# Kernel tuning notes

Measured on AMD Instinct MI355X. Metric: run time of the kernel, lower is better.

## Reference

```python
import jax, jax.numpy as jnp
import numpy as np

BLOCK_H = 32  # block_h from init
BLOCK_W = 32  # block_w from init


def _block_pool(mask, bh, bw):
    # mask: [H, S, S] int -> block mask [H, S//bh, S//bw] bool
    # Equivalent to the grouped Conv2d with all-ones kernel, stride=(bh,bw), then >0.
    H, S1, S2 = mask.shape
    m = mask.reshape(H, S1 // bh, bh, S2 // bw, bw).astype(jnp.float32)
    return m.sum(axis=(2, 4)) > 0


def _expand_block_mask(bm, bh, bw):
    # bm: [H, Nb_r, Nb_c] bool -> element mask [H, S, S] bool
    H, nr, nc = bm.shape
    e = jnp.broadcast_to(bm[:, :, None, :, None], (H, nr, bh, nc, bw))
    return e.reshape(H, nr * bh, nc * bw)


def setup_inputs() -> dict:
    key = jax.random.key(0)
    kq, kk, kv, km = jax.random.split(key, 4)
    Z, H, S, D = 1, 16, 2048, 64
    query = jax.random.normal(kq, (Z, H, S, D), dtype=jnp.float32)
    key_t = jax.random.normal(kk, (Z, H, S, D), dtype=jnp.float32)
    value = jax.random.normal(kv, (Z, H, S, D), dtype=jnp.float32)
    mask = jax.random.randint(km, (H, S, S), 0, 2, dtype=jnp.int32)
    return {"query": query, "key": key_t, "value": value, "mask": mask}


def reference(query, key, value, mask):
    # Dense equivalent of: sdd QK^T on layout blocks -> blocksparse causal
    # softmax (scale=1.0) -> dsd AV. Rows with no active blocks yield zeros,
    # matching the blocksparse representation (absent blocks contribute 0).
    H, S, _ = mask.shape
    bm = _block_pool(mask, BLOCK_H, BLOCK_W)              # [H, Nb, Nb]
    elem = _expand_block_mask(bm, BLOCK_H, BLOCK_W)       # [H, S, S]
    causal = jnp.tril(jnp.ones((S, S), dtype=bool))       # is_causal=True
    full = elem & causal                                  # [H, S, S]
    scale = 1.0                                           # scale=1.0 in forward

    scores = jnp.einsum('zhqd,zhkd->zhqk', query, key) * scale
    neg = jnp.asarray(-1e30, dtype=scores.dtype)
    scores = jnp.where(full[None], scores, neg)
    probs = jax.nn.softmax(scores, axis=-1)
    row_valid = jnp.any(full, axis=-1)                    # [H, S]
    probs = jnp.where(row_valid[None, :, :, None], probs, 0.0)
    out = jnp.einsum('zhqk,zhkd->zhqd', probs, value)
    return out
```

## Files before the change

### kernel.cpp

```cpp
#include <hip/hip_runtime.h>
#include <stdint.h>


#define HH 16
#define SS 2048
#define DD 64

using f32x4  = __attribute__((ext_vector_type(4))) float;
using s16x8  = __attribute__((ext_vector_type(8))) short;
using s16x4  = __attribute__((ext_vector_type(4))) short;
using f16x8  = __attribute__((ext_vector_type(8))) _Float16;

#define AS1 __attribute__((address_space(1)))
#define AS3 __attribute__((address_space(3)))

__device__ __forceinline__ unsigned short f2bf(float f) {
  unsigned u = __builtin_bit_cast(unsigned, f);
  u += 0x7fffu + ((u >> 16) & 1u);
  return (unsigned short)(u >> 16);
}
__device__ __forceinline__ float bf2f(unsigned short u) {
  return __builtin_bit_cast(float, ((unsigned)u) << 16);
}

__device__ __forceinline__ f32x4 mfma16bf16(s16x4 a, s16x4 b, f32x4 c) {
  return __builtin_amdgcn_mfma_f32_16x16x16bf16_1k(a, b, c, 0, 0, 0);
}

__global__ __launch_bounds__(256) void prep_kernel(
    const int* __restrict__ mask, const float* __restrict__ K,
    const float* __restrict__ V, unsigned char* __restrict__ bmask,
    unsigned short* __restrict__ Kf, unsigned short* __restrict__ Vtb) {
  __shared__ float tile[64][65];
  const int wg = blockIdx.x;
  const int t  = threadIdx.x;
  if (wg < 256) {
    const int tid = wg * 256 + t;
    {
      const int h = tid >> 12, br = (tid >> 6) & 63, bc = tid & 63;
      const int4* p = (const int4*)(mask + ((size_t)(h * SS + br * 32) * SS + bc * 32));
      int acc = 0;
#pragma unroll
      for (int i = 0; i < 8; ++i) { int4 v = p[i]; acc |= v.x | v.y | v.z | v.w; }
      if (acc == 0) {
        for (int r = 1; r < 32; ++r) {
          const int4* q2 = (const int4*)(mask + ((size_t)(h * SS + br * 32 + r) * SS + bc * 32));
          int a2 = 0;
#pragma unroll
          for (int i = 0; i < 8; ++i) { int4 v = q2[i]; a2 |= v.x | v.y | v.z | v.w; }
          acc |= a2;
          if (acc) break;
        }
      }
      bmask[tid] = acc != 0 ? 1 : 0;
    }
    {
      const float4* K4 = (const float4*)K;
      ushort4* Kf4 = (ushort4*)Kf;
#pragma unroll
      for (int i = 0; i < 8; ++i) {
        float4 v = K4[(size_t)i * 65536 + tid];
        ushort4 o;
        o.x = __builtin_bit_cast(unsigned short, (_Float16)v.x);
        o.y = __builtin_bit_cast(unsigned short, (_Float16)v.y);
        o.z = __builtin_bit_cast(unsigned short, (_Float16)v.z);
        o.w = __builtin_bit_cast(unsigned short, (_Float16)v.w);
        Kf4[(size_t)i * 65536 + tid] = o;
      }
    }
  } else {
    const int w2 = wg - 256;
    const int h = w2 >> 5, kt = w2 & 31;
    const float4* V4 = (const float4*)V;
#pragma unroll
    for (int j2 = 0; j2 < 4; ++j2) {
      int fi = t + j2 * 256;
      int row = fi >> 4, c4 = (fi & 15) * 4;
      float4 v = V4[(size_t)(h * SS + kt * 64 + row) * 16 + (fi & 15)];
      tile[row][c4] = v.x; tile[row][c4+1] = v.y; tile[row][c4+2] = v.z; tile[row][c4+3] = v.w;
    }
    __syncthreads();
    const int d = t >> 2, ks = (t & 3) * 16;
#pragma unroll
    for (int c = 0; c < 4; ++c) {
      ushort4 o;
      o.x = f2bf(tile[ks + c*4 + 0][d]);
      o.y = f2bf(tile[ks + c*4 + 1][d]);
      o.z = f2bf(tile[ks + c*4 + 2][d]);
      o.w = f2bf(tile[ks + c*4 + 3][d]);
      ((ushort4*)Vtb)[((size_t)(h * 64 + d) * SS + kt * 64 + ks + c*4) >> 2] = o;
    }
  }
}

__global__ __launch_bounds__(512, 1) void attn_kernel(
    const float* __restrict__ Q, const unsigned char* __restrict__ bmask,
    const unsigned short* __restrict__ Kf, const unsigned short* __restrict__ Vtb,
    float* __restrict__ O) {
  const int id = blockIdx.x;
  const int h  = id & 15;
  const int p  = id >> 4;

  const int t    = threadIdx.x;
  const int wave = t >> 6, lane = t & 63;
  const int n16  = lane & 15, quad = lane >> 4;
  const int wsub = wave & 3;
  const int qb   = (wave < 4) ? p : (31 - p);
  const int lastkt = 31 - p;

  __shared__ __align__(16) short ldsKV[16384];

  const int srow = t >> 3;
  const int c8   = (t & 7) ^ (srow & 7);
  const unsigned short* gk = Kf + (size_t)h * SS * DD + srow * DD + c8 * 8;
  const unsigned short* gv = Vtb + ((size_t)(h * 64 + srow)) * SS + c8 * 8;
  const int lofs = t * 8;
  auto stage = [&](int kt, int buf) {
    short* kb = ldsKV + buf * 8192;
    __builtin_amdgcn_global_load_lds((const AS1 void*)(gk + kt * 4096),
                                     (AS3 void*)(kb + lofs), 16, 0, 0);
    __builtin_amdgcn_global_load_lds((const AS1 void*)(gv + kt * 64),
                                     (AS3 void*)(kb + 4096 + lofs), 16, 0, 0);
  };

  const int qi0 = qb * 64 + wsub * 16;
  f16x8 qf[2];
  {
    const float* qp = Q + ((size_t)(h * SS + qi0 + n16)) * DD + quad * 8;
#pragma unroll
    for (int kc = 0; kc < 2; ++kc) {
      float4 a = *(const float4*)(qp + kc * 32);
      float4 b = *(const float4*)(qp + kc * 32 + 4);
      f16x8 f;
      f[0] = (_Float16)a.x; f[1] = (_Float16)a.y;
      f[2] = (_Float16)a.z; f[3] = (_Float16)a.w;
      f[4] = (_Float16)b.x; f[5] = (_Float16)b.y;
      f[6] = (_Float16)b.z; f[7] = (_Float16)b.w;
      qf[kc] = f;
    }
  }

  const int qbr = qb * 2 + (wsub >> 1);
  const unsigned long long bmw = __ballot(bmask[(h << 12) + (qbr << 6) + lane] != 0);

  float l_i = 0.f;
  f32x4 oa[4];
#pragma unroll
  for (int dt = 0; dt < 4; ++dt) oa[dt] = f32x4{0.f, 0.f, 0.f, 0.f};

  const int qi = qi0 + n16;

  stage(0, 0);
  for (int kt = 0; kt <= lastkt; ++kt) {
    __syncthreads();
    if (kt < lastkt) stage(kt + 1, (kt + 1) & 1);

    if (kt <= qb) {
      const short* khb = ldsKV + (kt & 1) * 8192;
      const short* vbase = khb + 4096;

      f32x4 S[4];
#pragma unroll
      for (int nb = 0; nb < 4; ++nb) S[nb] = f32x4{0.f, 0.f, 0.f, 0.f};
#pragma unroll
      for (int kc = 0; kc < 2; ++kc) {
#pragma unroll
        for (int nb = 0; nb < 4; ++nb) {
          int row = nb * 16 + n16;
          int pc  = (kc * 4 + quad) ^ (row & 7);
          f16x8 kh = __builtin_bit_cast(f16x8, *(const s16x8*)(khb + row * 64 + pc * 8));
          S[nb] = __builtin_amdgcn_mfma_f32_16x16x32_f16(kh, qf[kc], S[nb], 0, 0, 0);
        }
      }

      const int b0 = (int)((bmw >> (kt * 2)) & 1ull);
      const int b1 = (int)((bmw >> (kt * 2 + 1)) & 1ull);
      if ((kt == qb) | !(b0 & b1)) {
#pragma unroll
        for (int nb = 0; nb < 4; ++nb) {
          int bb = (nb < 2) ? b0 : b1;
          int k0 = kt * 64 + nb * 16 + quad * 4;
#pragma unroll
          for (int r = 0; r < 4; ++r) {
            bool ok = (k0 + r <= qi) && (bb != 0);
            S[nb][r] = ok ? S[nb][r] : -__builtin_inff();
          }
        }
      }

#pragma unroll
      for (int nb = 0; nb < 4; ++nb) {
        s16x4 pb;
#pragma unroll
        for (int r = 0; r < 4; ++r) {
          float pv = __expf(S[nb][r]);
          unsigned short pq = f2bf(pv);
          pb[r] = (short)pq;
          l_i += bf2f(pq);
        }
#pragma unroll
        for (int dt = 0; dt < 4; ++dt) {
          int row = dt * 16 + n16;
          int cc  = ((nb * 2) + (quad >> 1)) ^ (row & 7);
          s16x4 vv = *(const s16x4*)(vbase + row * 64 + cc * 8 + (quad & 1) * 4);
          oa[dt] = mfma16bf16(vv, pb, oa[dt]);
        }
      }
    }
  }

  {
    float lsum = l_i;
    lsum += __shfl_xor(lsum, 16);
    lsum += __shfl_xor(lsum, 32);
    float inv = lsum > 0.f ? 1.f / lsum : 0.f;
    float* op = O + ((size_t)(h * SS + qi)) * DD + quad * 4;
#pragma unroll
    for (int dt = 0; dt < 4; ++dt) {
      f32x4 o = oa[dt];
      float4 st = {o[0] * inv, o[1] * inv, o[2] * inv, o[3] * inv};
      *(float4*)(op + dt * 16) = st;
    }
  }
}

extern "C" void kernel_launch(void* const* d_in, const int* in_sizes, int n_in,
                              void* d_out, int out_size, void* d_ws, size_t ws_size,
                              hipStream_t stream) {
  const float* Q   = (const float*)d_in[0];
  const float* K   = (const float*)d_in[1];
  const float* V   = (const float*)d_in[2];
  const int* mask  = (const int*)d_in[3];
  float* out       = (float*)d_out;

  unsigned char* bmask = (unsigned char*)d_ws;
  unsigned short* Kf   = (unsigned short*)((char*)d_ws + 65536);
  unsigned short* Vtb  = (unsigned short*)((char*)d_ws + 65536 + 4194304);

  prep_kernel<<<768, 256, 0, stream>>>(mask, K, V, bmask, Kf, Vtb);
  attn_kernel<<<256, 512, 0, stream>>>(Q, bmask, Kf, Vtb, out);
}
```

Before: 341.2 us.

## Replace paired causal q-block workgroups with one q-block per 256-thread workgroup

```diff
diff --git a/kernel.cpp b/kernel.cpp
--- a/kernel.cpp
+++ b/kernel.cpp
@@ -21,6 +21,11 @@
 }
 __device__ __forceinline__ float bf2f(unsigned short u) {
   return __builtin_bit_cast(float, ((unsigned)u) << 16);
+}
+__device__ __forceinline__ void drain_all() {
+#if __has_builtin(__builtin_amdgcn_s_waitcnt)
+  __builtin_amdgcn_s_waitcnt(0);
+#endif
 }
 
 __device__ __forceinline__ f32x4 mfma16bf16(s16x4 a, s16x4 b, f32x4 c) {
@@ -93,37 +98,39 @@
   }
 }
 
-__global__ __launch_bounds__(512, 1) void attn_kernel(
+__global__ __launch_bounds__(256) void attn_kernel(
     const float* __restrict__ Q, const unsigned char* __restrict__ bmask,
     const unsigned short* __restrict__ Kf, const unsigned short* __restrict__ Vtb,
     float* __restrict__ O) {
   const int id = blockIdx.x;
   const int h  = id & 15;
-  const int p  = id >> 4;
+  const int qb = 31 - (id >> 4);
 
   const int t    = threadIdx.x;
   const int wave = t >> 6, lane = t & 63;
   const int n16  = lane & 15, quad = lane >> 4;
-  const int wsub = wave & 3;
-  const int qb   = (wave < 4) ? p : (31 - p);
-  const int lastkt = 31 - p;
 
   __shared__ __align__(16) short ldsKV[16384];
 
-  const int srow = t >> 3;
-  const int c8   = (t & 7) ^ (srow & 7);
-  const unsigned short* gk = Kf + (size_t)h * SS * DD + srow * DD + c8 * 8;
-  const unsigned short* gv = Vtb + ((size_t)(h * 64 + srow)) * SS + c8 * 8;
-  const int lofs = t * 8;
   auto stage = [&](int kt, int buf) {
     short* kb = ldsKV + buf * 8192;
-    __builtin_amdgcn_global_load_lds((const AS1 void*)(gk + kt * 4096),
-                                     (AS3 void*)(kb + lofs), 16, 0, 0);
-    __builtin_amdgcn_global_load_lds((const AS1 void*)(gv + kt * 64),
-                                     (AS3 void*)(kb + 4096 + lofs), 16, 0, 0);
+#pragma unroll
+    for (int i = 0; i < 2; ++i) {
+      int slot = i * 256 + t;
+      int row  = slot >> 3;
+      int c8   = (slot & 7) ^ (row & 7);
+      const unsigned short* gk =
+          Kf + (size_t)h * SS * DD + (size_t)(kt * 64 + row) * DD + c8 * 8;
+      __builtin_amdgcn_global_load_lds((const AS1 void*)gk,
+                                       (AS3 void*)(kb + slot * 8), 16, 0, 0);
+      const unsigned short* gv =
+          Vtb + ((size_t)(h * 64 + row)) * SS + kt * 64 + c8 * 8;
+      __builtin_amdgcn_global_load_lds((const AS1 void*)gv,
+                                       (AS3 void*)(kb + 4096 + slot * 8), 16, 0, 0);
+    }
   };
 
-  const int qi0 = qb * 64 + wsub * 16;
+  const int qi0 = qb * 64 + wave * 16;
   f16x8 qf[2];
   {
     const float* qp = Q + ((size_t)(h * SS + qi0 + n16)) * DD + quad * 8;
@@ -140,7 +147,7 @@
     }
   }
 
-  const int qbr = qb * 2 + (wsub >> 1);
+  const int qbr = qb * 2 + (wave >> 1);
   const unsigned long long bmw = __ballot(bmask[(h << 12) + (qbr << 6) + lane] != 0);
 
   float l_i = 0.f;
@@ -151,60 +158,59 @@
   const int qi = qi0 + n16;
 
   stage(0, 0);
-  for (int kt = 0; kt <= lastkt; ++kt) {
+  for (int kt = 0; kt <= qb; ++kt) {
+    drain_all();
     __syncthreads();
-    if (kt < lastkt) stage(kt + 1, (kt + 1) & 1);
-
-    if (kt <= qb) {
-      const short* khb = ldsKV + (kt & 1) * 8192;
-      const short* vbase = khb + 4096;
-
-      f32x4 S[4];
-#pragma unroll
-      for (int nb = 0; nb < 4; ++nb) S[nb] = f32x4{0.f, 0.f, 0.f, 0.f};
-#pragma unroll
-      for (int kc = 0; kc < 2; ++kc) {
-#pragma unroll
-        for (int nb = 0; nb < 4; ++nb) {
-          int row = nb * 16 + n16;
-          int pc  = (kc * 4 + quad) ^ (row & 7);
-          f16x8 kh = __builtin_bit_cast(f16x8, *(const s16x8*)(khb + row * 64 + pc * 8));
-          S[nb] = __builtin_amdgcn_mfma_f32_16x16x32_f16(kh, qf[kc], S[nb], 0, 0, 0);
+    if (kt < qb) stage(kt + 1, (kt + 1) & 1);
+
+    const short* khb = ldsKV + (kt & 1) * 8192;
+    const short* vbase = khb + 4096;
+
+    f32x4 S[4];
+#pragma unroll
+    for (int nb = 0; nb < 4; ++nb) S[nb] = f32x4{0.f, 0.f, 0.f, 0.f};
+#pragma unroll
+    for (int kc = 0; kc < 2; ++kc) {
+#pragma unroll
+      for (int nb = 0; nb < 4; ++nb) {
+        int row = nb * 16 + n16;
+        int pc  = (kc * 4 + quad) ^ (row & 7);
+        f16x8 kh = __builtin_bit_cast(f16x8, *(const s16x8*)(khb + row * 64 + pc * 8));
+        S[nb] = __builtin_amdgcn_mfma_f32_16x16x32_f16(kh, qf[kc], S[nb], 0, 0, 0);
+      }
+    }
+
+    const int b0 = (int)((bmw >> (kt * 2)) & 1ull);
+    const int b1 = (int)((bmw >> (kt * 2 + 1)) & 1ull);
+    if ((kt == qb) | !(b0 & b1)) {
+#pragma unroll
+      for (int nb = 0; nb < 4; ++nb) {
+        int bb = (nb < 2) ? b0 : b1;
+        int k0 = kt * 64 + nb * 16 + quad * 4;
+#pragma unroll
+        for (int r = 0; r < 4; ++r) {
+          bool ok = (k0 + r <= qi) && (bb != 0);
+          S[nb][r] = ok ? S[nb][r] : -__builtin_inff();
         }
       }
-
-      const int b0 = (int)((bmw >> (kt * 2)) & 1ull);
-      const int b1 = (int)((bmw >> (kt * 2 + 1)) & 1ull);
-      if ((kt == qb) | !(b0 & b1)) {
-#pragma unroll
-        for (int nb = 0; nb < 4; ++nb) {
-          int bb = (nb < 2) ? b0 : b1;
-          int k0 = kt * 64 + nb * 16 + quad * 4;
-#pragma unroll
-          for (int r = 0; r < 4; ++r) {
-            bool ok = (k0 + r <= qi) && (bb != 0);
-            S[nb][r] = ok ? S[nb][r] : -__builtin_inff();
-          }
-        }
-      }
-
-#pragma unroll
-      for (int nb = 0; nb < 4; ++nb) {
-        s16x4 pb;
-#pragma unroll
-        for (int r = 0; r < 4; ++r) {
-          float pv = __expf(S[nb][r]);
-          unsigned short pq = f2bf(pv);
-          pb[r] = (short)pq;
-          l_i += bf2f(pq);
-        }
-#pragma unroll
-        for (int dt = 0; dt < 4; ++dt) {
-          int row = dt * 16 + n16;
-          int cc  = ((nb * 2) + (quad >> 1)) ^ (row & 7);
-          s16x4 vv = *(const s16x4*)(vbase + row * 64 + cc * 8 + (quad & 1) * 4);
-          oa[dt] = mfma16bf16(vv, pb, oa[dt]);
-        }
+    }
+
+#pragma unroll
+    for (int nb = 0; nb < 4; ++nb) {
+      s16x4 pb;
+#pragma unroll
+      for (int r = 0; r < 4; ++r) {
+        float pv = __expf(S[nb][r]);
+        unsigned short pq = f2bf(pv);
+        pb[r] = (short)pq;
+        l_i += bf2f(pq);
+      }
+#pragma unroll
+      for (int dt = 0; dt < 4; ++dt) {
+        int row = dt * 16 + n16;
+        int cc  = ((nb * 2) + (quad >> 1)) ^ (row & 7);
+        s16x4 vv = *(const s16x4*)(vbase + row * 64 + cc * 8 + (quad & 1) * 4);
+        oa[dt] = mfma16bf16(vv, pb, oa[dt]);
       }
     }
   }
@@ -238,5 +244,5 @@
   unsigned short* Vtb  = (unsigned short*)((char*)d_ws + 65536 + 4194304);
 
   prep_kernel<<<768, 256, 0, stream>>>(mask, K, V, bmask, Kf, Vtb);
-  attn_kernel<<<256, 512, 0, stream>>>(Q, bmask, Kf, Vtb, out);
-}
+  attn_kernel<<<512, 256, 0, stream>>>(Q, bmask, Kf, Vtb, out);
+}
```

Result: no change. 343.9 us (+0.8%).
